# Kernel tuning notes

Measured on AMD Instinct MI355X. Metric: run time of the kernel, lower is better.

The kernel has to match this reference:

```python
import jax, jax.numpy as jnp
import numpy as np

NUM_HEADS = 16
KEY_DIM = 64
D_MODEL = NUM_HEADS * KEY_DIM
BATCH = 2
SEQ = 2048


def _rope_tables(seq_len, dim, dtype):
    # matches RotaryPositionalEmbedding: inv_freq = exp(arange(0,dim,2) * (-ln(10000)/dim))
    pos = jnp.arange(seq_len, dtype=dtype)                      # [S]
    inv_freq = jnp.exp(jnp.arange(0, dim, 2, dtype=dtype) * (-np.log(10000.0) / dim))  # [D/2]
    angles = pos[:, None] * inv_freq[None, :]                   # [S, D/2]
    return jnp.sin(angles), jnp.cos(angles)


def _apply_rope(x, sin, cos):
    # x: [B, S, H, D]; sin/cos: [S, D/2] broadcast over batch and heads
    sin = sin[None, :, None, :]
    cos = cos[None, :, None, :]
    x1, x2 = jnp.split(x, 2, axis=-1)
    return jnp.concatenate([cos * x1 - sin * x2, sin * x1 + cos * x2], axis=-1)


def setup_inputs() -> dict:
    key = jax.random.key(0)
    ks = jax.random.split(key, 5)
    s = 1.0 / np.sqrt(D_MODEL)
    return {
        "inputs": jax.random.normal(ks[0], (BATCH, SEQ, D_MODEL), jnp.float32),
        "Wq": jax.random.normal(ks[1], (D_MODEL, D_MODEL), jnp.float32) * s,
        "bq": jnp.zeros((D_MODEL,), jnp.float32),
        "Wk": jax.random.normal(ks[2], (D_MODEL, D_MODEL), jnp.float32) * s,
        "bk": jnp.zeros((D_MODEL,), jnp.float32),
        "Wv": jax.random.normal(ks[3], (D_MODEL, D_MODEL), jnp.float32) * s,
        "bv": jnp.zeros((D_MODEL,), jnp.float32),
        "Wo": jax.random.normal(ks[4], (D_MODEL, D_MODEL), jnp.float32) * s,
        "bo": jnp.zeros((D_MODEL,), jnp.float32),
    }


def reference(inputs, Wq, bq, Wk, bk, Wv, bv, Wo, bo):
    B, S, _ = inputs.shape
    # QKV projections, split into heads: [B, S, H, Dk]
    q = (inputs @ Wq + bq).reshape(B, S, NUM_HEADS, KEY_DIM)
    k = (inputs @ Wk + bk).reshape(B, S, NUM_HEADS, KEY_DIM)
    v = (inputs @ Wv + bv).reshape(B, S, NUM_HEADS, KEY_DIM)
    # rotary embedding on q/k (per-head dim = KEY_DIM)
    sin, cos = _rope_tables(S, KEY_DIM, inputs.dtype)
    q = _apply_rope(q, sin, cos)
    k = _apply_rope(k, sin, cos)
    # attention: [B, H, S, S]
    scores = jnp.einsum("bshd,bthd->bhst", q, k) / jnp.sqrt(
        jnp.asarray(KEY_DIM, inputs.dtype))
    weights = jax.nn.softmax(scores, axis=-1)  # dropout inactive (training=False)
    ctx = jnp.einsum("bhst,bthd->bshd", weights, v).reshape(B, S, D_MODEL)
    return ctx @ Wo + bo
```

## Files before the change

kernel.cpp:

```cpp
#include <hip/hip_runtime.h>
#include <math.h>

#define NH 16
#define KD 64
#define DMODEL 1024
#define BATCH 2
#define SEQ 2048
#define MROWS (BATCH*SEQ)

typedef float f32x4 __attribute__((ext_vector_type(4)));
typedef __bf16 bf16x8 __attribute__((ext_vector_type(8)));

__device__ __forceinline__ unsigned short f2bf(float x) {
    union { float f; unsigned u; } a; a.f = x;
    unsigned r = a.u + 0x7fffu + ((a.u >> 16) & 1u);
    return (unsigned short)(r >> 16);
}
__device__ __forceinline__ unsigned cvt_pk_bf16(float lo, float hi) {
    unsigned r;
    asm("v_cvt_pk_bf16_f32 %0, %1, %2" : "=v"(r) : "v"(lo), "v"(hi));
    return r;
}
__device__ __forceinline__ float exp2_hw(float x) {
    float r;
    asm("v_exp_f32 %0, %1" : "=v"(r) : "v"(x));
    return r;
}

__device__ __forceinline__ void gl2lds16(const void* gsrc, void* ldst) {
    __builtin_amdgcn_global_load_lds(
        (const __attribute__((address_space(1))) void*)gsrc,
        (__attribute__((address_space(3))) void*)ldst, 16, 0, 0);
}

__global__ __launch_bounds__(256) void k_prep(const float* __restrict__ x,
                                              const float* __restrict__ W0,
                                              const float* __restrict__ W1,
                                              const float* __restrict__ W2,
                                              const float* __restrict__ W3,
                                              float* __restrict__ sin_t,
                                              float* __restrict__ cos_t,
                                              unsigned short* __restrict__ xh,
                                              unsigned short* __restrict__ Th) {
    __shared__ float L[64][65];
    const int bid = blockIdx.x;
    const int tid = threadIdx.x;
    if (bid < 256) {
        int idx = bid * 256 + tid;
        int s = idx >> 5, i = idx & 31;
        float invf = expf((float)(2 * i) * (-logf(10000.0f) / (float)KD));
        float ang = (float)s * invf;
        sin_t[idx] = sinf(ang);
        cos_t[idx] = cosf(ang);
        return;
    }
    if (bid < 4352) {
        int idx = (bid - 256) * 256 + tid;
        float4 v = reinterpret_cast<const float4*>(x)[idx];
        ushort4 h;
        h.x = f2bf(v.x); h.y = f2bf(v.y); h.z = f2bf(v.z); h.w = f2bf(v.w);
        reinterpret_cast<ushort4*>(xh)[idx] = h;
        return;
    }
    int r = bid - 4352;
    int z = r >> 8;
    int rr = r & 255;
    const int n0 = (rr & 15) * 64, k0 = (rr >> 4) * 64;
    const float* W = (z == 0) ? W0 : (z == 1) ? W1 : (z == 2) ? W2 : W3;
    const size_t zoff = (size_t)z * DMODEL * DMODEL;
#pragma unroll
    for (int it = 0; it < 4; ++it) {
        int idx = tid + it * 256;
        int rw = idx >> 4;
        int c4 = (idx & 15) * 4;
        float4 v = *reinterpret_cast<const float4*>(&W[(size_t)(k0 + rw) * DMODEL + n0 + c4]);
        L[rw][c4 + 0] = v.x; L[rw][c4 + 1] = v.y; L[rw][c4 + 2] = v.z; L[rw][c4 + 3] = v.w;
    }
    __syncthreads();
    int rn = tid >> 2;
    int ks = (tid & 3) * 16;
#pragma unroll
    for (int g = 0; g < 4; ++g) {
        ushort4 h;
        h.x = f2bf(L[ks + g * 4 + 0][rn]);
        h.y = f2bf(L[ks + g * 4 + 1][rn]);
        h.z = f2bf(L[ks + g * 4 + 2][rn]);
        h.w = f2bf(L[ks + g * 4 + 3][rn]);
        size_t o = zoff + (size_t)(n0 + rn) * DMODEL + k0 + ks + g * 4;
        *reinterpret_cast<ushort4*>(&Th[o]) = h;
    }
}

__global__ __launch_bounds__(256) void k_mgemm_qkv(const unsigned short* __restrict__ Ah_g,
                                                   const unsigned short* __restrict__ Wp,
                                                   const float* __restrict__ bq,
                                                   const float* __restrict__ bk,
                                                   const float* __restrict__ bv,
                                                   unsigned short* __restrict__ qh_,
                                                   unsigned short* __restrict__ kh_,
                                                   unsigned short* __restrict__ vth,
                                                   const float* __restrict__ sin_t,
                                                   const float* __restrict__ cos_t) {
    __shared__ unsigned short Ah[2][128 * 64];
    __shared__ unsigned short Bh[2][64 * 64];
    const int tid = threadIdx.x;
    const int lane = tid & 63;
    const int w = tid >> 6;

    int bid = blockIdx.x;
    int wg = (bid & 7) * 192 + (bid >> 3);
    const int z = wg >> 9;
    const int r = wg & 511;
    const int m0 = (r >> 4) * 128;
    const int n0 = (r & 15) * 64;
    const unsigned short* Bh_g = Wp + (size_t)z * DMODEL * DMODEL;
    const float* bias = (z == 0) ? bq : (z == 1) ? bk : bv;

    size_t a_goff[4]; int a_ldst[4];
#pragma unroll
    for (int it = 0; it < 4; ++it) {
        int off = it * 4096 + w * 1024 + lane * 16;
        int row = off >> 7;
        int pg = (off >> 4) & 7;
        int lg = pg ^ (row & 7);
        a_goff[it] = (size_t)(m0 + row) * DMODEL + lg * 8;
        a_ldst[it] = it * 2048 + w * 512;
    }
    size_t b_goff[2]; int b_ldst[2];
#pragma unroll
    for (int it = 0; it < 2; ++it) {
        int off = it * 4096 + w * 1024 + lane * 16;
        int row = off >> 7;
        int pg = (off >> 4) & 7;
        int lg = pg ^ (row & 7);
        b_goff[it] = (size_t)(n0 + row) * DMODEL + lg * 8;
        b_ldst[it] = it * 2048 + w * 512;
    }

    int aoff[2][2], boff[4][2];
#pragma unroll
    for (int mf = 0; mf < 2; ++mf)
#pragma unroll
        for (int ks = 0; ks < 2; ++ks) {
            int row = w * 32 + mf * 16 + (lane & 15);
            int g = ks * 4 + (lane >> 4);
            aoff[mf][ks] = row * 64 + ((g ^ (row & 7)) * 8);
        }
#pragma unroll
    for (int nf = 0; nf < 4; ++nf)
#pragma unroll
        for (int ks = 0; ks < 2; ++ks) {
            int row = nf * 16 + (lane & 15);
            int g = ks * 4 + (lane >> 4);
            boff[nf][ks] = row * 64 + ((g ^ (row & 7)) * 8);
        }

    f32x4 acc[2][4];
#pragma unroll
    for (int mf = 0; mf < 2; ++mf)
#pragma unroll
        for (int nf = 0; nf < 4; ++nf) acc[mf][nf] = (f32x4){0.f, 0.f, 0.f, 0.f};

#define STAGEG(BUF, KT) do {                                                  \
        int k0_ = (KT) * 64;                                                  \
        gl2lds16(Ah_g + a_goff[0] + k0_, &Ah[BUF][a_ldst[0]]);                \
        gl2lds16(Ah_g + a_goff[1] + k0_, &Ah[BUF][a_ldst[1]]);                \
        gl2lds16(Ah_g + a_goff[2] + k0_, &Ah[BUF][a_ldst[2]]);                \
        gl2lds16(Ah_g + a_goff[3] + k0_, &Ah[BUF][a_ldst[3]]);                \
        gl2lds16(Bh_g + b_goff[0] + k0_, &Bh[BUF][b_ldst[0]]);                \
        gl2lds16(Bh_g + b_goff[1] + k0_, &Bh[BUF][b_ldst[1]]);                \
    } while (0)

    STAGEG(0, 0);

    for (int kt = 0; kt < 16; ++kt) {
        const int cur = kt & 1;
        asm volatile("s_waitcnt vmcnt(0)" ::: "memory");
        __builtin_amdgcn_s_barrier();
        if (kt < 15) STAGEG(cur ^ 1, kt + 1);
#pragma unroll
        for (int ks = 0; ks < 2; ++ks) {
            bf16x8 ah[2], bh[4];
#pragma unroll
            for (int mf = 0; mf < 2; ++mf)
                ah[mf] = *reinterpret_cast<const bf16x8*>(&Ah[cur][aoff[mf][ks]]);
#pragma unroll
            for (int nf = 0; nf < 4; ++nf)
                bh[nf] = *reinterpret_cast<const bf16x8*>(&Bh[cur][boff[nf][ks]]);
#pragma unroll
            for (int mf = 0; mf < 2; ++mf)
#pragma unroll
                for (int nf = 0; nf < 4; ++nf)
                    acc[mf][nf] = __builtin_amdgcn_mfma_f32_16x16x32_bf16(ah[mf], bh[nf], acc[mf][nf], 0, 0, 0);
        }
    }
#undef STAGEG

    const int c = lane & 15;
    const int rq = lane >> 4;
    float bv_[4];
#pragma unroll
    for (int nf = 0; nf < 4; ++nf) bv_[nf] = bias[n0 + nf * 16 + c];

#pragma unroll
    for (int mf = 0; mf < 2; ++mf) {
        int mbase = m0 + w * 32 + mf * 16 + rq * 4;
        if (z < 2) {
#pragma unroll
            for (int r2 = 0; r2 < 4; ++r2) {
                int m = mbase + r2;
                int srow = m & (SEQ - 1);
                float x0 = acc[mf][0][r2] + bv_[0];
                float x1 = acc[mf][1][r2] + bv_[1];
                float x2 = acc[mf][2][r2] + bv_[2];
                float x3 = acc[mf][3][r2] + bv_[3];
                float s0 = sin_t[srow * 32 + c],      c0 = cos_t[srow * 32 + c];
                float s1 = sin_t[srow * 32 + 16 + c], c1 = cos_t[srow * 32 + 16 + c];
                float o0 = c0 * x0 - s0 * x2;
                float o2 = s0 * x0 + c0 * x2;
                float o1 = c1 * x1 - s1 * x3;
                float o3 = s1 * x1 + c1 * x3;
                unsigned short* Ohi = kh_;
                if (z == 0) {
                    const float qs = 0.18033688011112042f;
                    o0 *= qs; o1 *= qs; o2 *= qs; o3 *= qs;
                    Ohi = qh_;
                }
                float ov[4] = { o0, o1, o2, o3 };
                size_t base = (size_t)m * DMODEL + n0 + c;
#pragma unroll
                for (int nf = 0; nf < 4; ++nf)
                    Ohi[base + nf * 16] = f2bf(ov[nf]);
            }
        } else {
            int bb = mbase >> 11;
            int s = mbase & (SEQ - 1);
            int h = n0 >> 6;
#pragma unroll
            for (int nf = 0; nf < 4; ++nf) {
                ushort4 h4;
                float v0 = acc[mf][nf][0] + bv_[nf];
                float v1 = acc[mf][nf][1] + bv_[nf];
                float v2 = acc[mf][nf][2] + bv_[nf];
                float v3 = acc[mf][nf][3] + bv_[nf];
                h4.x = f2bf(v0); h4.y = f2bf(v1); h4.z = f2bf(v2); h4.w = f2bf(v3);
                int d = nf * 16 + c;
                size_t o = ((size_t)((bb * NH + h) * KD + d)) * SEQ + s;
                *reinterpret_cast<ushort4*>(&vth[o]) = h4;
            }
        }
    }
}

__global__ __launch_bounds__(256) void k_mgemm_o(const unsigned short* __restrict__ Ah_g,
                                                 const unsigned short* __restrict__ Bh_g,
                                                 const float* __restrict__ bias,
                                                 float* __restrict__ Cf) {
    __shared__ unsigned short Ah[2][128 * 64];
    __shared__ unsigned short Bh[2][64 * 64];
    const int tid = threadIdx.x;
    const int lane = tid & 63;
    const int w = tid >> 6;

    int bid = blockIdx.x;
    int wg = (bid & 7) * 64 + (bid >> 3);
    const int m0 = (wg >> 4) * 128;
    const int n0 = (wg & 15) * 64;

    size_t a_goff[4]; int a_ldst[4];
#pragma unroll
    for (int it = 0; it < 4; ++it) {
        int off = it * 4096 + w * 1024 + lane * 16;
        int row = off >> 7;
        int pg = (off >> 4) & 7;
        int lg = pg ^ (row & 7);
        a_goff[it] = (size_t)(m0 + row) * DMODEL + lg * 8;
        a_ldst[it] = it * 2048 + w * 512;
    }
    size_t b_goff[2]; int b_ldst[2];
#pragma unroll
    for (int it = 0; it < 2; ++it) {
        int off = it * 4096 + w * 1024 + lane * 16;
        int row = off >> 7;
        int pg = (off >> 4) & 7;
        int lg = pg ^ (row & 7);
        b_goff[it] = (size_t)(n0 + row) * DMODEL + lg * 8;
        b_ldst[it] = it * 2048 + w * 512;
    }

    int aoff[2][2], boff[4][2];
#pragma unroll
    for (int mf = 0; mf < 2; ++mf)
#pragma unroll
        for (int ks = 0; ks < 2; ++ks) {
            int row = w * 32 + mf * 16 + (lane & 15);
            int g = ks * 4 + (lane >> 4);
            aoff[mf][ks] = row * 64 + ((g ^ (row & 7)) * 8);
        }
#pragma unroll
    for (int nf = 0; nf < 4; ++nf)
#pragma unroll
        for (int ks = 0; ks < 2; ++ks) {
            int row = nf * 16 + (lane & 15);
            int g = ks * 4 + (lane >> 4);
            boff[nf][ks] = row * 64 + ((g ^ (row & 7)) * 8);
        }

    f32x4 acc[2][4];
#pragma unroll
    for (int mf = 0; mf < 2; ++mf)
#pragma unroll
        for (int nf = 0; nf < 4; ++nf) acc[mf][nf] = (f32x4){0.f, 0.f, 0.f, 0.f};

#define STAGEG(BUF, KT) do {                                                  \
        int k0_ = (KT) * 64;                                                  \
        gl2lds16(Ah_g + a_goff[0] + k0_, &Ah[BUF][a_ldst[0]]);                \
        gl2lds16(Ah_g + a_goff[1] + k0_, &Ah[BUF][a_ldst[1]]);                \
        gl2lds16(Ah_g + a_goff[2] + k0_, &Ah[BUF][a_ldst[2]]);                \
        gl2lds16(Ah_g + a_goff[3] + k0_, &Ah[BUF][a_ldst[3]]);                \
        gl2lds16(Bh_g + b_goff[0] + k0_, &Bh[BUF][b_ldst[0]]);                \
        gl2lds16(Bh_g + b_goff[1] + k0_, &Bh[BUF][b_ldst[1]]);                \
    } while (0)

    STAGEG(0, 0);

    for (int kt = 0; kt < 16; ++kt) {
        const int cur = kt & 1;
        asm volatile("s_waitcnt vmcnt(0)" ::: "memory");
        __builtin_amdgcn_s_barrier();
        if (kt < 15) STAGEG(cur ^ 1, kt + 1);
#pragma unroll
        for (int ks = 0; ks < 2; ++ks) {
            bf16x8 ah[2], bh[4];
#pragma unroll
            for (int mf = 0; mf < 2; ++mf)
                ah[mf] = *reinterpret_cast<const bf16x8*>(&Ah[cur][aoff[mf][ks]]);
#pragma unroll
            for (int nf = 0; nf < 4; ++nf)
                bh[nf] = *reinterpret_cast<const bf16x8*>(&Bh[cur][boff[nf][ks]]);
#pragma unroll
            for (int mf = 0; mf < 2; ++mf)
#pragma unroll
                for (int nf = 0; nf < 4; ++nf)
                    acc[mf][nf] = __builtin_amdgcn_mfma_f32_16x16x32_bf16(ah[mf], bh[nf], acc[mf][nf], 0, 0, 0);
        }
    }
#undef STAGEG

    const int c = lane & 15;
    const int rq = lane >> 4;
    float bv[4];
#pragma unroll
    for (int nf = 0; nf < 4; ++nf) bv[nf] = bias[n0 + nf * 16 + c];
#pragma unroll
    for (int mf = 0; mf < 2; ++mf) {
        int mbase = m0 + w * 32 + mf * 16 + rq * 4;
#pragma unroll
        for (int nf = 0; nf < 4; ++nf)
#pragma unroll
            for (int r = 0; r < 4; ++r)
                Cf[(size_t)(mbase + r) * DMODEL + n0 + nf * 16 + c] = acc[mf][nf][r] + bv[nf];
    }
}

__global__ __launch_bounds__(256) void k_attn(const unsigned short* __restrict__ qhi,
                                              const unsigned short* __restrict__ khi,
                                              const unsigned short* __restrict__ vthi,
                                              unsigned short* __restrict__ ch) {
    __shared__ unsigned short Kh[2][64 * 64];
    __shared__ unsigned short Vh[3][64 * 64];
    __shared__ unsigned short Ps[4][32 * 64];

    const int tid  = threadIdx.x;
    const int lane = tid & 63;
    const int w    = tid >> 6;

    int bid = blockIdx.x;
    int wg  = (bid & 7) * 64 + (bid >> 3);
    const int qt = wg & 15;
    const int h  = (wg >> 4) & 15;
    const int b  = wg >> 8;
    const int q0 = qt * 128;

    bf16x8 qf[2][2];
#pragma unroll
    for (int mf = 0; mf < 2; ++mf)
#pragma unroll
        for (int ks = 0; ks < 2; ++ks) {
            int row = q0 + w * 32 + mf * 16 + (lane & 15);
            int d = ks * 32 + (lane >> 4) * 8;
            qf[mf][ks] = *reinterpret_cast<const bf16x8*>(
                qhi + ((size_t)(b * SEQ + row) * NH + h) * KD + d);
        }

    size_t gK[2], gV[2]; int ld_[2];
#pragma unroll
    for (int it = 0; it < 2; ++it) {
        int off = it * 4096 + tid * 16;
        int row = off >> 7;
        int pg = (off >> 4) & 7;
        int lg = pg ^ (row & 7);
        gK[it] = ((size_t)(b * SEQ + row) * NH + h) * KD + lg * 8;
        gV[it] = ((size_t)(b * NH + h) * KD + row) * SEQ + lg * 8;
        ld_[it] = it * 2048 + w * 512;
    }

    f32x4 acc[2][4];
    float l_part[2] = { 0.f, 0.f };
#pragma unroll
    for (int mf = 0; mf < 2; ++mf)
#pragma unroll
        for (int nf = 0; nf < 4; ++nf) acc[mf][nf] = (f32x4){0.f, 0.f, 0.f, 0.f};

#define STAGE(KB, VB, TT) do {                                               \
        size_t kadv = (size_t)(TT) * 64 * NH * KD;                           \
        size_t vadv = (size_t)(TT) * 64;                                     \
        gl2lds16(khi  + gK[0] + kadv, &Kh[KB][ld_[0]]);                      \
        gl2lds16(khi  + gK[1] + kadv, &Kh[KB][ld_[1]]);                      \
        gl2lds16(vthi + gV[0] + vadv, &Vh[VB][ld_[0]]);                      \
        gl2lds16(vthi + gV[1] + vadv, &Vh[VB][ld_[1]]);                      \
    } while (0)

#define PV_STEP(VSRC) do {                                                   \
        _Pragma("unroll")                                                    \
        for (int ks = 0; ks < 2; ++ks) {                                     \
            bf16x8 pa[2];                                                    \
            _Pragma("unroll")                                                \
            for (int mf = 0; mf < 2; ++mf) {                                 \
                int prow = mf * 16 + (lane & 15);                            \
                int aoff = prow * 64 + (((ks * 4 + (lane >> 4)) ^ (prow & 7)) * 8); \
                pa[mf] = *reinterpret_cast<const bf16x8*>(&Ps[w][aoff]);     \
            }                                                                \
            _Pragma("unroll")                                                \
            for (int nf = 0; nf < 4; ++nf) {                                 \
                int drow = nf * 16 + (lane & 15);                            \
                int voff = drow * 64 + (((ks * 4 + (lane >> 4)) ^ (drow & 7)) * 8); \
                bf16x8 vf = *reinterpret_cast<const bf16x8*>(&Vh[VSRC][voff]); \
                _Pragma("unroll")                                            \
                for (int mf = 0; mf < 2; ++mf)                               \
                    acc[mf][nf] = __builtin_amdgcn_mfma_f32_16x16x32_bf16(pa[mf], vf, acc[mf][nf], 0, 0, 0); \
            }                                                                \
        }                                                                    \
    } while (0)

    STAGE(0, 0, 0);

    int vnext = 1;
    int vprev = 2;

    for (int t = 0; t < 32; ++t) {
        const int ck = t & 1;
        asm volatile("s_waitcnt vmcnt(0)" ::: "memory");
        __builtin_amdgcn_s_barrier();
        if (t < 31) STAGE(ck ^ 1, vnext, t + 1);

        __builtin_amdgcn_s_setprio(1);
        f32x4 s[2][4];
#pragma unroll
        for (int mf = 0; mf < 2; ++mf)
#pragma unroll
            for (int nf = 0; nf < 4; ++nf) s[mf][nf] = (f32x4){0.f, 0.f, 0.f, 0.f};
#pragma unroll
        for (int nf = 0; nf < 4; ++nf) {
#pragma unroll
            for (int ks = 0; ks < 2; ++ks) {
                int trow = nf * 16 + (lane & 15);
                int koff = trow * 64 + (((ks * 4 + (lane >> 4)) ^ (trow & 7)) * 8);
                bf16x8 kf = *reinterpret_cast<const bf16x8*>(&Kh[ck][koff]);
#pragma unroll
                for (int mf = 0; mf < 2; ++mf)
                    s[mf][nf] = __builtin_amdgcn_mfma_f32_16x16x32_bf16(kf, qf[mf][ks], s[mf][nf], 0, 0, 0);
            }
        }
        if (t > 0) PV_STEP(vprev);
        __builtin_amdgcn_s_setprio(0);

#pragma unroll
        for (int mf = 0; mf < 2; ++mf) {
            int qloc = mf * 16 + (lane & 15);
#pragma unroll
            for (int nf = 0; nf < 4; ++nf) {
                float p0 = exp2_hw(s[mf][nf][0]);
                float p1 = exp2_hw(s[mf][nf][1]);
                float p2 = exp2_hw(s[mf][nf][2]);
                float p3 = exp2_hw(s[mf][nf][3]);
                l_part[mf] += (p0 + p1) + (p2 + p3);
                unsigned w01 = cvt_pk_bf16(p0, p1);
                unsigned w23 = cvt_pk_bf16(p2, p3);
                int tb = nf * 16 + (lane >> 4) * 4;
                int phys = tb ^ ((qloc & 7) << 3);
                *reinterpret_cast<uint2*>(&Ps[w][qloc * 64 + phys]) = make_uint2(w01, w23);
            }
        }

        vnext = (vnext == 2) ? 0 : vnext + 1;
        vprev = (vprev == 2) ? 0 : vprev + 1;
    }

    PV_STEP(vprev);
#undef PV_STEP
#undef STAGE

#pragma unroll
    for (int mf = 0; mf < 2; ++mf) {
        l_part[mf] += __shfl_xor(l_part[mf], 16);
        l_part[mf] += __shfl_xor(l_part[mf], 32);
    }
#pragma unroll
    for (int mf = 0; mf < 2; ++mf) {
#pragma unroll
        for (int r = 0; r < 4; ++r) {
            float lsum = __shfl(l_part[mf], (lane >> 4) * 4 + r);
            float inv = 1.0f / lsum;
            int qg = q0 + w * 32 + mf * 16 + (lane >> 4) * 4 + r;
#pragma unroll
            for (int nf = 0; nf < 4; ++nf) {
                int d = nf * 16 + (lane & 15);
                float val = acc[mf][nf][r] * inv;
                ch[((size_t)(b * SEQ + qg) * NH + h) * KD + d] = f2bf(val);
            }
        }
    }
}

extern "C" void kernel_launch(void* const* d_in, const int* in_sizes, int n_in,
                              void* d_out, int out_size, void* d_ws, size_t ws_size,
                              hipStream_t stream) {
    const float* x  = (const float*)d_in[0];
    const float* Wq = (const float*)d_in[1];
    const float* bq = (const float*)d_in[2];
    const float* Wk = (const float*)d_in[3];
    const float* bk = (const float*)d_in[4];
    const float* Wv = (const float*)d_in[5];
    const float* bv = (const float*)d_in[6];
    const float* Wo = (const float*)d_in[7];
    const float* bo = (const float*)d_in[8];
    float* out = (float*)d_out;

    const size_t NE = (size_t)MROWS * DMODEL;
    const size_t WE = (size_t)DMODEL * DMODEL;
    float* ws    = (float*)d_ws;
    float* sin_t = ws;
    float* cos_t = sin_t + SEQ * 32;
    unsigned short* p = (unsigned short*)(cos_t + SEQ * 32);
    unsigned short* xh   = p; p += NE;
    unsigned short* qh_  = p; p += NE;
    unsigned short* kh_  = p; p += NE;
    unsigned short* vth  = p; p += NE;
    unsigned short* wth  = p; p += 4 * WE;
    unsigned short* ctxh = xh;

    k_prep<<<5376, 256, 0, stream>>>(x, Wq, Wk, Wv, Wo, sin_t, cos_t, xh, wth);

    k_mgemm_qkv<<<1536, 256, 0, stream>>>(xh, wth, bq, bk, bv, qh_, kh_, vth, sin_t, cos_t);

    k_attn<<<512, 256, 0, stream>>>(qh_, kh_, vth, ctxh);

    k_mgemm_o<<<512, 256, 0, stream>>>(ctxh, wth + 3 * WE, bo, out);
}
```

Baseline: 117.2 us.

## Load K/V fragments directly from global into registers, drop LDS staging

Removes the shared-memory double/triple buffering of K and V tiles. Each wave now loads its MFMA fragments for K and V straight from global memory into registers every iteration. The software-pipelined PV step is also replaced by an in-iteration PV after softmax. This drops LDS traffic and block barriers, but each of the 4 waves re-reads the same K/V from global/L2 without prefetch overlap, and register pressure rises.

```diff
diff --git a/kernel.cpp b/kernel.cpp
--- a/kernel.cpp
+++ b/kernel.cpp
@@ -367,8 +367,6 @@
                                               const unsigned short* __restrict__ khi,
                                               const unsigned short* __restrict__ vthi,
                                               unsigned short* __restrict__ ch) {
-    __shared__ unsigned short Kh[2][64 * 64];
-    __shared__ unsigned short Vh[3][64 * 64];
     __shared__ unsigned short Ps[4][32 * 64];
 
     const int tid  = threadIdx.x;
@@ -393,17 +391,10 @@
                 qhi + ((size_t)(b * SEQ + row) * NH + h) * KD + d);
         }
 
-    size_t gK[2], gV[2]; int ld_[2];
-#pragma unroll
-    for (int it = 0; it < 2; ++it) {
-        int off = it * 4096 + tid * 16;
-        int row = off >> 7;
-        int pg = (off >> 4) & 7;
-        int lg = pg ^ (row & 7);
-        gK[it] = ((size_t)(b * SEQ + row) * NH + h) * KD + lg * 8;
-        gV[it] = ((size_t)(b * NH + h) * KD + row) * SEQ + lg * 8;
-        ld_[it] = it * 2048 + w * 512;
-    }
+    const unsigned short* kb = khi + ((size_t)b * SEQ * NH + h) * KD
+                               + (size_t)(lane & 15) * (NH * KD) + ((lane >> 4) * 8);
+    const unsigned short* vb = vthi + ((size_t)(b * NH + h) * KD + (lane & 15)) * SEQ
+                               + ((lane >> 4) * 8);
 
     f32x4 acc[2][4];
     float l_part[2] = { 0.f, 0.f };
@@ -412,47 +403,19 @@
 #pragma unroll
         for (int nf = 0; nf < 4; ++nf) acc[mf][nf] = (f32x4){0.f, 0.f, 0.f, 0.f};
 
-#define STAGE(KB, VB, TT) do {                                               \
-        size_t kadv = (size_t)(TT) * 64 * NH * KD;                           \
-        size_t vadv = (size_t)(TT) * 64;                                     \
-        gl2lds16(khi  + gK[0] + kadv, &Kh[KB][ld_[0]]);                      \
-        gl2lds16(khi  + gK[1] + kadv, &Kh[KB][ld_[1]]);                      \
-        gl2lds16(vthi + gV[0] + vadv, &Vh[VB][ld_[0]]);                      \
-        gl2lds16(vthi + gV[1] + vadv, &Vh[VB][ld_[1]]);                      \
-    } while (0)
-
-#define PV_STEP(VSRC) do {                                                   \
-        _Pragma("unroll")                                                    \
-        for (int ks = 0; ks < 2; ++ks) {                                     \
-            bf16x8 pa[2];                                                    \
-            _Pragma("unroll")                                                \
-            for (int mf = 0; mf < 2; ++mf) {                                 \
-                int prow = mf * 16 + (lane & 15);                            \
-                int aoff = prow * 64 + (((ks * 4 + (lane >> 4)) ^ (prow & 7)) * 8); \
-                pa[mf] = *reinterpret_cast<const bf16x8*>(&Ps[w][aoff]);     \
-            }                                                                \
-            _Pragma("unroll")                                                \
-            for (int nf = 0; nf < 4; ++nf) {                                 \
-                int drow = nf * 16 + (lane & 15);                            \
-                int voff = drow * 64 + (((ks * 4 + (lane >> 4)) ^ (drow & 7)) * 8); \
-                bf16x8 vf = *reinterpret_cast<const bf16x8*>(&Vh[VSRC][voff]); \
-                _Pragma("unroll")                                            \
-                for (int mf = 0; mf < 2; ++mf)                               \
-                    acc[mf][nf] = __builtin_amdgcn_mfma_f32_16x16x32_bf16(pa[mf], vf, acc[mf][nf], 0, 0, 0); \
-            }                                                                \
-        }                                                                    \
-    } while (0)
-
-    STAGE(0, 0, 0);
-
-    int vnext = 1;
-    int vprev = 2;
-
     for (int t = 0; t < 32; ++t) {
-        const int ck = t & 1;
-        asm volatile("s_waitcnt vmcnt(0)" ::: "memory");
-        __builtin_amdgcn_s_barrier();
-        if (t < 31) STAGE(ck ^ 1, vnext, t + 1);
+        const int t0 = t * 64;
+
+        bf16x8 kf[4][2], vf[4][2];
+#pragma unroll
+        for (int nf = 0; nf < 4; ++nf)
+#pragma unroll
+            for (int ks = 0; ks < 2; ++ks) {
+                kf[nf][ks] = *reinterpret_cast<const bf16x8*>(
+                    kb + (size_t)(t0 + nf * 16) * (NH * KD) + ks * 32);
+                vf[nf][ks] = *reinterpret_cast<const bf16x8*>(
+                    vb + (size_t)(nf * 16) * SEQ + t0 + ks * 32);
+            }
 
         __builtin_amdgcn_s_setprio(1);
         f32x4 s[2][4];
@@ -461,18 +424,12 @@
 #pragma unroll
             for (int nf = 0; nf < 4; ++nf) s[mf][nf] = (f32x4){0.f, 0.f, 0.f, 0.f};
 #pragma unroll
-        for (int nf = 0; nf < 4; ++nf) {
-#pragma unroll
-            for (int ks = 0; ks < 2; ++ks) {
-                int trow = nf * 16 + (lane & 15);
-                int koff = trow * 64 + (((ks * 4 + (lane >> 4)) ^ (trow & 7)) * 8);
-                bf16x8 kf = *reinterpret_cast<const bf16x8*>(&Kh[ck][koff]);
+        for (int nf = 0; nf < 4; ++nf)
+#pragma unroll
+            for (int ks = 0; ks < 2; ++ks)
 #pragma unroll
                 for (int mf = 0; mf < 2; ++mf)
-                    s[mf][nf] = __builtin_amdgcn_mfma_f32_16x16x32_bf16(kf, qf[mf][ks], s[mf][nf], 0, 0, 0);
-            }
-        }
-        if (t > 0) PV_STEP(vprev);
+                    s[mf][nf] = __builtin_amdgcn_mfma_f32_16x16x32_bf16(kf[nf][ks], qf[mf][ks], s[mf][nf], 0, 0, 0);
         __builtin_amdgcn_s_setprio(0);
 
 #pragma unroll
@@ -493,13 +450,24 @@
             }
         }
 
-        vnext = (vnext == 2) ? 0 : vnext + 1;
-        vprev = (vprev == 2) ? 0 : vprev + 1;
-    }
-
-    PV_STEP(vprev);
-#undef PV_STEP
-#undef STAGE
+        __builtin_amdgcn_s_setprio(1);
+#pragma unroll
+        for (int ks = 0; ks < 2; ++ks) {
+            bf16x8 pa[2];
+#pragma unroll
+            for (int mf = 0; mf < 2; ++mf) {
+                int prow = mf * 16 + (lane & 15);
+                int aoff = prow * 64 + (((ks * 4 + (lane >> 4)) ^ (prow & 7)) * 8);
+                pa[mf] = *reinterpret_cast<const bf16x8*>(&Ps[w][aoff]);
+            }
+#pragma unroll
+            for (int nf = 0; nf < 4; ++nf)
+#pragma unroll
+                for (int mf = 0; mf < 2; ++mf)
+                    acc[mf][nf] = __builtin_amdgcn_mfma_f32_16x16x32_bf16(pa[mf], vf[nf][ks], acc[mf][nf], 0, 0, 0);
+        }
+        __builtin_amdgcn_s_setprio(0);
+    }
 
 #pragma unroll
     for (int mf = 0; mf < 2; ++mf) {
```

New measurement: 183.7 us. 56.8% more time.

## Compute Q, K and V tiles in one block to share the staged input tile

Applied to the files above, without the earlier changes.

The QKV GEMM kernel now has each workgroup compute all three projections for its 128x64 output tile. It loads the activation tile into LDS once and stages three weight tiles, instead of launching separate blocks per projection that each reload the same activation tile. This cuts activation global/LDS traffic to a third and shrinks the grid from 1536 to 512 blocks. In exchange it triples the accumulator registers and raises LDS use from 48KB to 80KB, which may lower occupancy and leave the 256-CU GPU with only two waves of blocks.

```diff
diff --git a/kernel.cpp b/kernel.cpp
--- a/kernel.cpp
+++ b/kernel.cpp
@@ -102,19 +102,16 @@
                                                    const float* __restrict__ sin_t,
                                                    const float* __restrict__ cos_t) {
     __shared__ unsigned short Ah[2][128 * 64];
-    __shared__ unsigned short Bh[2][64 * 64];
+    __shared__ unsigned short Bh[2][3][64 * 64];
     const int tid = threadIdx.x;
     const int lane = tid & 63;
     const int w = tid >> 6;
 
     int bid = blockIdx.x;
-    int wg = (bid & 7) * 192 + (bid >> 3);
-    const int z = wg >> 9;
-    const int r = wg & 511;
-    const int m0 = (r >> 4) * 128;
-    const int n0 = (r & 15) * 64;
-    const unsigned short* Bh_g = Wp + (size_t)z * DMODEL * DMODEL;
-    const float* bias = (z == 0) ? bq : (z == 1) ? bk : bv;
+    int wg = (bid & 7) * 64 + (bid >> 3);
+    const int m0 = (wg >> 4) * 128;
+    const int n0 = (wg & 15) * 64;
+    const size_t WE = (size_t)DMODEL * DMODEL;
 
     size_t a_goff[4]; int a_ldst[4];
 #pragma unroll
@@ -155,11 +152,13 @@
             boff[nf][ks] = row * 64 + ((g ^ (row & 7)) * 8);
         }
 
-    f32x4 acc[2][4];
-#pragma unroll
-    for (int mf = 0; mf < 2; ++mf)
-#pragma unroll
-        for (int nf = 0; nf < 4; ++nf) acc[mf][nf] = (f32x4){0.f, 0.f, 0.f, 0.f};
+    f32x4 acc[3][2][4];
+#pragma unroll
+    for (int z = 0; z < 3; ++z)
+#pragma unroll
+        for (int mf = 0; mf < 2; ++mf)
+#pragma unroll
+            for (int nf = 0; nf < 4; ++nf) acc[z][mf][nf] = (f32x4){0.f, 0.f, 0.f, 0.f};
 
 #define STAGEG(BUF, KT) do {                                                  \
         int k0_ = (KT) * 64;                                                  \
@@ -167,8 +166,12 @@
         gl2lds16(Ah_g + a_goff[1] + k0_, &Ah[BUF][a_ldst[1]]);                \
         gl2lds16(Ah_g + a_goff[2] + k0_, &Ah[BUF][a_ldst[2]]);                \
         gl2lds16(Ah_g + a_goff[3] + k0_, &Ah[BUF][a_ldst[3]]);                \
-        gl2lds16(Bh_g + b_goff[0] + k0_, &Bh[BUF][b_ldst[0]]);                \
-        gl2lds16(Bh_g + b_goff[1] + k0_, &Bh[BUF][b_ldst[1]]);                \
+        gl2lds16(Wp + 0 * WE + b_goff[0] + k0_, &Bh[BUF][0][b_ldst[0]]);      \
+        gl2lds16(Wp + 0 * WE + b_goff[1] + k0_, &Bh[BUF][0][b_ldst[1]]);      \
+        gl2lds16(Wp + 1 * WE + b_goff[0] + k0_, &Bh[BUF][1][b_ldst[0]]);      \
+        gl2lds16(Wp + 1 * WE + b_goff[1] + k0_, &Bh[BUF][1][b_ldst[1]]);      \
+        gl2lds16(Wp + 2 * WE + b_goff[0] + k0_, &Bh[BUF][2][b_ldst[0]]);      \
+        gl2lds16(Wp + 2 * WE + b_goff[1] + k0_, &Bh[BUF][2][b_ldst[1]]);      \
     } while (0)
 
     STAGEG(0, 0);
@@ -180,51 +183,60 @@
         if (kt < 15) STAGEG(cur ^ 1, kt + 1);
 #pragma unroll
         for (int ks = 0; ks < 2; ++ks) {
-            bf16x8 ah[2], bh[4];
+            bf16x8 ah[2];
 #pragma unroll
             for (int mf = 0; mf < 2; ++mf)
                 ah[mf] = *reinterpret_cast<const bf16x8*>(&Ah[cur][aoff[mf][ks]]);
 #pragma unroll
-            for (int nf = 0; nf < 4; ++nf)
-                bh[nf] = *reinterpret_cast<const bf16x8*>(&Bh[cur][boff[nf][ks]]);
-#pragma unroll
-            for (int mf = 0; mf < 2; ++mf)
+            for (int z = 0; z < 3; ++z) {
+                bf16x8 bh[4];
 #pragma unroll
                 for (int nf = 0; nf < 4; ++nf)
-                    acc[mf][nf] = __builtin_amdgcn_mfma_f32_16x16x32_bf16(ah[mf], bh[nf], acc[mf][nf], 0, 0, 0);
+                    bh[nf] = *reinterpret_cast<const bf16x8*>(&Bh[cur][z][boff[nf][ks]]);
+#pragma unroll
+                for (int mf = 0; mf < 2; ++mf)
+#pragma unroll
+                    for (int nf = 0; nf < 4; ++nf)
+                        acc[z][mf][nf] = __builtin_amdgcn_mfma_f32_16x16x32_bf16(ah[mf], bh[nf], acc[z][mf][nf], 0, 0, 0);
+            }
         }
     }
 #undef STAGEG
 
     const int c = lane & 15;
     const int rq = lane >> 4;
-    float bv_[4];
-#pragma unroll
-    for (int nf = 0; nf < 4; ++nf) bv_[nf] = bias[n0 + nf * 16 + c];
+    float bvq[4], bvk[4], bvv[4];
+#pragma unroll
+    for (int nf = 0; nf < 4; ++nf) {
+        bvq[nf] = bq[n0 + nf * 16 + c];
+        bvk[nf] = bk[n0 + nf * 16 + c];
+        bvv[nf] = bv[n0 + nf * 16 + c];
+    }
 
 #pragma unroll
     for (int mf = 0; mf < 2; ++mf) {
         int mbase = m0 + w * 32 + mf * 16 + rq * 4;
-        if (z < 2) {
+#pragma unroll
+        for (int z = 0; z < 2; ++z) {
+            const float* bb_ = (z == 0) ? bvq : bvk;
+            unsigned short* Ohi = (z == 0) ? qh_ : kh_;
 #pragma unroll
             for (int r2 = 0; r2 < 4; ++r2) {
                 int m = mbase + r2;
                 int srow = m & (SEQ - 1);
-                float x0 = acc[mf][0][r2] + bv_[0];
-                float x1 = acc[mf][1][r2] + bv_[1];
-                float x2 = acc[mf][2][r2] + bv_[2];
-                float x3 = acc[mf][3][r2] + bv_[3];
+                float x0 = acc[z][mf][0][r2] + bb_[0];
+                float x1 = acc[z][mf][1][r2] + bb_[1];
+                float x2 = acc[z][mf][2][r2] + bb_[2];
+                float x3 = acc[z][mf][3][r2] + bb_[3];
                 float s0 = sin_t[srow * 32 + c],      c0 = cos_t[srow * 32 + c];
                 float s1 = sin_t[srow * 32 + 16 + c], c1 = cos_t[srow * 32 + 16 + c];
                 float o0 = c0 * x0 - s0 * x2;
                 float o2 = s0 * x0 + c0 * x2;
                 float o1 = c1 * x1 - s1 * x3;
                 float o3 = s1 * x1 + c1 * x3;
-                unsigned short* Ohi = kh_;
                 if (z == 0) {
                     const float qs = 0.18033688011112042f;
                     o0 *= qs; o1 *= qs; o2 *= qs; o3 *= qs;
-                    Ohi = qh_;
                 }
                 float ov[4] = { o0, o1, o2, o3 };
                 size_t base = (size_t)m * DMODEL + n0 + c;
@@ -232,17 +244,18 @@
                 for (int nf = 0; nf < 4; ++nf)
                     Ohi[base + nf * 16] = f2bf(ov[nf]);
             }
-        } else {
+        }
+        {
             int bb = mbase >> 11;
             int s = mbase & (SEQ - 1);
             int h = n0 >> 6;
 #pragma unroll
             for (int nf = 0; nf < 4; ++nf) {
                 ushort4 h4;
-                float v0 = acc[mf][nf][0] + bv_[nf];
-                float v1 = acc[mf][nf][1] + bv_[nf];
-                float v2 = acc[mf][nf][2] + bv_[nf];
-                float v3 = acc[mf][nf][3] + bv_[nf];
+                float v0 = acc[2][mf][nf][0] + bvv[nf];
+                float v1 = acc[2][mf][nf][1] + bvv[nf];
+                float v2 = acc[2][mf][nf][2] + bvv[nf];
+                float v3 = acc[2][mf][nf][3] + bvv[nf];
                 h4.x = f2bf(v0); h4.y = f2bf(v1); h4.z = f2bf(v2); h4.w = f2bf(v3);
                 int d = nf * 16 + c;
                 size_t o = ((size_t)((bb * NH + h) * KD + d)) * SEQ + s;
@@ -552,7 +565,7 @@
 
     k_prep<<<5376, 256, 0, stream>>>(x, Wq, Wk, Wv, Wo, sin_t, cos_t, xh, wth);
 
-    k_mgemm_qkv<<<1536, 256, 0, stream>>>(xh, wth, bq, bk, bv, qh_, kh_, vth, sin_t, cos_t);
+    k_mgemm_qkv<<<512, 256, 0, stream>>>(xh, wth, bq, bk, bv, qh_, kh_, vth, sin_t, cos_t);
 
     k_attn<<<512, 256, 0, stream>>>(qh_, kh_, vth, ctxh);
 
```

Measured after the change: 113.8 us. 1.03x faster.
